# Optimization experiments

Hardware: AMD Instinct MI355X
Metric: run time of the kernel (lower is better)

Reference implementation:

```python
import jax, jax.numpy as jnp
import numpy as np

EMBED_DIM = 512
NUM_HEADS = 8
D_HEAD = EMBED_DIM // NUM_HEADS  # 64
BLOCK = 64
SEQ = 8192
BATCH = 2
N_GLOBAL = 2
N_WINDOW = 3
N_RANDOM = 3
NB = SEQ // BLOCK  # 128 blocks
M = N_GLOBAL + N_WINDOW + N_RANDOM  # gathered key blocks per query block


def setup_inputs() -> dict:
    key = jax.random.key(0)
    ks = jax.random.split(key, 12)
    s = 0.05  # ~xavier scale for [512,64]
    return {
        "query": jax.random.normal(ks[0], (SEQ, BATCH, EMBED_DIM), jnp.float32),
        "key_inp": jax.random.normal(ks[1], (SEQ, BATCH, EMBED_DIM), jnp.float32),
        "value": jax.random.normal(ks[2], (SEQ, BATCH, EMBED_DIM), jnp.float32),
        "q_w": jax.random.normal(ks[3], (NUM_HEADS, EMBED_DIM, D_HEAD), jnp.float32) * s,
        "k_w": jax.random.normal(ks[4], (NUM_HEADS, EMBED_DIM, D_HEAD), jnp.float32) * s,
        "v_w": jax.random.normal(ks[5], (NUM_HEADS, EMBED_DIM, D_HEAD), jnp.float32) * s,
        "q_b": jnp.zeros((NUM_HEADS, D_HEAD), jnp.float32),
        "k_b": jnp.zeros((NUM_HEADS, D_HEAD), jnp.float32),
        "v_b": jnp.zeros((NUM_HEADS, D_HEAD), jnp.float32),
        "out_w": jax.random.normal(ks[6], (EMBED_DIM, EMBED_DIM), jnp.float32) * 0.04,
        "out_b": jnp.zeros((EMBED_DIM,), jnp.float32),
        "rand_idx": jax.random.randint(ks[7], (NB, N_RANDOM), 0, NB, dtype=jnp.int32),
    }


def _gather_block_idx(rand_idx):
    # per query block: global blocks + sliding window (mod NB) + random blocks -> [NB, M]
    glob = jnp.broadcast_to(jnp.arange(N_GLOBAL, dtype=jnp.int32), (NB, N_GLOBAL))
    half = N_WINDOW // 2
    win = (jnp.arange(NB, dtype=jnp.int32)[:, None]
           + jnp.arange(N_WINDOW, dtype=jnp.int32)[None, :] - half) % NB
    return jnp.concatenate([glob, win, rand_idx], axis=1)


def _sparse_attn(Q, K, V, rand_idx):
    # Q,K,V: [B,H,S,dh] -> out [B,H,S,dh]
    B, H, S, dh = Q.shape
    Qb = Q.reshape(B, H, NB, BLOCK, dh)
    Kb = K.reshape(B, H, NB, BLOCK, dh)
    Vb = V.reshape(B, H, NB, BLOCK, dh)
    idx = _gather_block_idx(rand_idx)              # [NB, M]
    Kg = Kb[:, :, idx]                              # [B,H,NB,M,BLOCK,dh]
    Vg = Vb[:, :, idx].reshape(B, H, NB, M * BLOCK, dh)
    scores = jnp.einsum('bhnqd,bhnmkd->bhnqmk', Qb, Kg) / jnp.sqrt(jnp.float32(dh))
    scores = scores.reshape(B, H, NB, BLOCK, M * BLOCK)
    attn = jax.nn.softmax(scores, axis=-1)
    out = jnp.einsum('bhnqk,bhnkd->bhnqd', attn, Vg)
    return out.reshape(B, H, S, dh)


def reference(query, key_inp, value, q_w, k_w, v_w, q_b, k_b, v_b, out_w, out_b, rand_idx):
    # batch_first=False: [S,B,E] -> [B,S,E]
    q = jnp.transpose(query, (1, 0, 2))
    k = jnp.transpose(key_inp, (1, 0, 2))
    v = jnp.transpose(value, (1, 0, 2))
    # per-head projections: [B,S,E] x [H,E,dh] -> [B,H,S,dh]
    Q = jnp.einsum('bse,hed->bhsd', q, q_w) + q_b[None, :, None, :]
    K = jnp.einsum('bse,hed->bhsd', k, k_w) + k_b[None, :, None, :]
    V = jnp.einsum('bse,hed->bhsd', v, v_w) + v_b[None, :, None, :]
    ao = _sparse_attn(Q, K, V, rand_idx)            # [B,H,S,dh]
    flat = jnp.transpose(ao, (0, 2, 1, 3)).reshape(BATCH * SEQ, EMBED_DIM)
    out = flat @ out_w.T + out_b                    # nn.Linear
    out = out.reshape(BATCH, SEQ, EMBED_DIM)
    return jnp.transpose(out, (1, 0, 2))            # back to [S,B,E]
```

## Files before the change

kernel.cpp:

```cpp
#include <hip/hip_runtime.h>
#include <stdint.h>

#define NBLK 128
#define KDIM 512

typedef __attribute__((ext_vector_type(8))) short short8;
typedef __attribute__((ext_vector_type(4))) float f32x4;
typedef unsigned short u16;

__device__ __forceinline__ u16 f2bf(float f) {
  unsigned u = __float_as_uint(f);
  u = u + 0x7fffu + ((u >> 16) & 1u);
  return (u16)(u >> 16);
}

__device__ __forceinline__ short8 pack8(float4 a, float4 b) {
  short8 r;
  r[0] = (short)f2bf(a.x); r[1] = (short)f2bf(a.y);
  r[2] = (short)f2bf(a.z); r[3] = (short)f2bf(a.w);
  r[4] = (short)f2bf(b.x); r[5] = (short)f2bf(b.y);
  r[6] = (short)f2bf(b.z); r[7] = (short)f2bf(b.w);
  return r;
}

__device__ __forceinline__ void g2l16(const void* g, void* l) {
  __builtin_amdgcn_global_load_lds(
      (__attribute__((address_space(1))) void*)(g),
      (__attribute__((address_space(3))) void*)(l), 16, 0, 0);
}

__global__ void prep_weights(const float* __restrict__ qw, const float* __restrict__ kw,
                             const float* __restrict__ vw, const float* __restrict__ ow,
                             u16* __restrict__ wqt, u16* __restrict__ wkt,
                             u16* __restrict__ wvt, u16* __restrict__ owb) {
  int t = blockIdx.x * 256 + threadIdx.x;
  int y = blockIdx.y;
  if (y < 3) {
    const float* w = (y == 0) ? qw : (y == 1) ? kw : vw;
    u16* dstp = (y == 0) ? wqt : (y == 1) ? wkt : wvt;
    int c = t >> 7;
    int e4 = (t & 127) * 4;
    int h = c >> 6, d = c & 63;
    const float* base = w + h * (512 * 64) + d;
    ushort4 r;
    r.x = f2bf(base[(e4 + 0) * 64]);
    r.y = f2bf(base[(e4 + 1) * 64]);
    r.z = f2bf(base[(e4 + 2) * 64]);
    r.w = f2bf(base[(e4 + 3) * 64]);
    *(ushort4*)(dstp + c * 512 + e4) = r;
  } else {
    float4 val = *(const float4*)(ow + t * 4);
    ushort4 r;
    r.x = f2bf(val.x); r.y = f2bf(val.y); r.z = f2bf(val.z); r.w = f2bf(val.w);
    *(ushort4*)(owb + t * 4) = r;
  }
}

template <int MODE, bool AF32, bool BF32>
__device__ __forceinline__ void gemm_core(const void* __restrict__ Av, const void* __restrict__ Bv,
                                          const float* __restrict__ bias, void* __restrict__ dstv,
                                          int tileM, int tileN, u16* sh) {
  const int t = threadIdx.x;
  const int lane = t & 63, w = t >> 6;
  const int l15 = lane & 15, quad = lane >> 4;
  const int wm = w >> 1, wn = w & 1;
  u16* As = sh;
  u16* Bs = sh + 4096;

  f32x4 acc[4][4];
#pragma unroll
  for (int i = 0; i < 4; ++i)
#pragma unroll
    for (int j = 0; j < 4; ++j) acc[i][j] = (f32x4){0.f, 0.f, 0.f, 0.f};

  const int r = t >> 1, h = t & 1;
  const int swz = (r >> 1) & 3;

  const float* gA32 = nullptr; const u16* gA16 = nullptr;
  {
    const int grow = tileM + r;
    if (AF32) {
      const int b = grow >> 13, s = grow & 8191;
      gA32 = (const float*)Av + (size_t)(s * 2 + b) * 512 + h * 16;
    } else {
      gA16 = (const u16*)Av + (size_t)grow * 512 + h * 16;
    }
  }
  const float* gB32 = nullptr; const u16* gB16 = nullptr;
  {
    const int grow = tileN + r;
    if (BF32) {
      const int b = grow >> 13, s = grow & 8191;
      gB32 = (const float*)Bv + (size_t)(s * 2 + b) * 512 + h * 16;
    } else {
      gB16 = (const u16*)Bv + (size_t)grow * 512 + h * 16;
    }
  }

  u16* ldsA = As + r * 32;
  u16* ldsB = Bs + r * 32;
  const int p0 = ((2 * h) ^ swz) << 3;
  const int p1 = ((2 * h + 1) ^ swz) << 3;

  float4 fa[4], fb[4];
  short8 sa[2], sb[2];

#define LOAD_TILE(k0)                                             \
  do {                                                            \
    if (AF32) {                                                   \
      fa[0] = *(const float4*)(gA32 + (k0));                      \
      fa[1] = *(const float4*)(gA32 + (k0) + 4);                  \
      fa[2] = *(const float4*)(gA32 + (k0) + 8);                  \
      fa[3] = *(const float4*)(gA32 + (k0) + 12);                 \
    } else {                                                      \
      sa[0] = *(const short8*)(gA16 + (k0));                      \
      sa[1] = *(const short8*)(gA16 + (k0) + 8);                  \
    }                                                             \
    if (BF32) {                                                   \
      fb[0] = *(const float4*)(gB32 + (k0));                      \
      fb[1] = *(const float4*)(gB32 + (k0) + 4);                  \
      fb[2] = *(const float4*)(gB32 + (k0) + 8);                  \
      fb[3] = *(const float4*)(gB32 + (k0) + 12);                 \
    } else {                                                      \
      sb[0] = *(const short8*)(gB16 + (k0));                      \
      sb[1] = *(const short8*)(gB16 + (k0) + 8);                  \
    }                                                             \
  } while (0)

#define STORE_TILE()                                              \
  do {                                                            \
    if (AF32) {                                                   \
      *(short8*)(ldsA + p0) = pack8(fa[0], fa[1]);                \
      *(short8*)(ldsA + p1) = pack8(fa[2], fa[3]);                \
    } else {                                                      \
      *(short8*)(ldsA + p0) = sa[0];                              \
      *(short8*)(ldsA + p1) = sa[1];                              \
    }                                                             \
    if (BF32) {                                                   \
      *(short8*)(ldsB + p0) = pack8(fb[0], fb[1]);                \
      *(short8*)(ldsB + p1) = pack8(fb[2], fb[3]);                \
    } else {                                                      \
      *(short8*)(ldsB + p0) = sb[0];                              \
      *(short8*)(ldsB + p1) = sb[1];                              \
    }                                                             \
  } while (0)

  LOAD_TILE(0);
  STORE_TILE();
  __syncthreads();

  for (int k0 = 0; k0 < KDIM; k0 += 32) {
    const bool has_next = (k0 + 32 < KDIM);
    if (has_next) LOAD_TILE(k0 + 32);

    short8 af[4], bf[4];
#pragma unroll
    for (int mt = 0; mt < 4; ++mt) {
      const int ra = wm * 64 + mt * 16 + l15;
      af[mt] = *(const short8*)(As + ra * 32 + ((quad ^ ((ra >> 1) & 3)) << 3));
    }
#pragma unroll
    for (int nt = 0; nt < 4; ++nt) {
      const int rb = wn * 64 + nt * 16 + l15;
      bf[nt] = *(const short8*)(Bs + rb * 32 + ((quad ^ ((rb >> 1) & 3)) << 3));
    }
#pragma unroll
    for (int mt = 0; mt < 4; ++mt)
#pragma unroll
      for (int nt = 0; nt < 4; ++nt)
        acc[mt][nt] = __builtin_amdgcn_mfma_f32_16x16x32_bf16(af[mt], bf[nt], acc[mt][nt], 0, 0, 0);

    if (has_next) {
      __syncthreads();
      STORE_TILE();
      __syncthreads();
    }
  }
#undef LOAD_TILE
#undef STORE_TILE
  __syncthreads();

  if (MODE == 0 || MODE == 1) {
#pragma unroll
    for (int mt = 0; mt < 4; ++mt)
#pragma unroll
      for (int nt = 0; nt < 4; ++nt)
#pragma unroll
        for (int rr = 0; rr < 4; ++rr) {
          const int lrow = wm * 64 + mt * 16 + quad * 4 + rr;
          const int col = wn * 64 + nt * 16 + l15;
          float v = acc[mt][nt][rr] + (MODE == 0 ? bias[tileN + col] : bias[tileM + lrow]);
          const int ch = col >> 3;
          sh[lrow * 128 + ((ch ^ (lrow & 7)) << 3) + (col & 7)] = f2bf(v);
        }
    __syncthreads();
#pragma unroll
    for (int p = 0; p < 8; ++p) {
      const int idx = p * 256 + t;
      const int row = idx >> 4, c = idx & 15;
      short8 vch = *(const short8*)(sh + row * 128 + ((c ^ (row & 7)) << 3));
      if (MODE == 0) {
        const int m = tileM + row, b = m >> 13, s = m & 8191;
        const int n0 = tileN + c * 8, hh = n0 >> 6, d = n0 & 63;
        *(short8*)((u16*)dstv + (((b * 8 + hh) * 8192 + s) * 64 + d)) = vch;
      } else {
        const int hd = tileM + row;
        const int n0 = tileN + c * 8, b = n0 >> 13, s = n0 & 8191;
        *(short8*)((u16*)dstv + ((b * 512 + hd) * 8192 + s)) = vch;
      }
    }
  } else {
    float* Cf = (float*)sh;
#pragma unroll
    for (int half = 0; half < 2; ++half) {
      if (wm == half) {
#pragma unroll
        for (int mt = 0; mt < 4; ++mt)
#pragma unroll
          for (int nt = 0; nt < 4; ++nt)
#pragma unroll
            for (int rr = 0; rr < 4; ++rr) {
              const int lrow = mt * 16 + quad * 4 + rr;
              const int col = wn * 64 + nt * 16 + l15;
              float v = acc[mt][nt][rr] + bias[tileN + col];
              const int ch = col >> 2;
              Cf[lrow * 128 + ((ch ^ ((lrow & 7) << 2)) << 2) + (col & 3)] = v;
            }
      }
      __syncthreads();
#pragma unroll
      for (int p = 0; p < 8; ++p) {
        const int idx = p * 256 + t;
        const int row = idx >> 5, c = idx & 31;
        float4 v4 = *(const float4*)(Cf + row * 128 + ((c ^ ((row & 7) << 2)) << 2));
        const int m = tileM + half * 64 + row;
        const int s = m & 8191, b = m >> 13;
        *(float4*)((float*)dstv + ((s * 2 + b) * 512 + tileN + c * 4)) = v4;
      }
      __syncthreads();
    }
  }
}

__global__ __launch_bounds__(256, 4)
void gemm_qkv(const float* __restrict__ q, const float* __restrict__ k, const float* __restrict__ v,
              const u16* __restrict__ WqT, const u16* __restrict__ WkT, const u16* __restrict__ WvT,
              const float* __restrict__ qbi, const float* __restrict__ kbi, const float* __restrict__ vbi,
              u16* __restrict__ Qb, u16* __restrict__ Kb, u16* __restrict__ Vt) {
  __shared__ u16 sh[16384];
  const int id = blockIdx.x + blockIdx.y * 4;
  const int xs = (id >> 3) & 3;
  const int ys = (id & 7) * 16 + (id >> 5);
  const int z = blockIdx.z;
  if (z == 0)      gemm_core<0, true, false>(q, WqT, qbi, Qb, ys * 128, xs * 128, sh);
  else if (z == 1) gemm_core<0, true, false>(k, WkT, kbi, Kb, ys * 128, xs * 128, sh);
  else             gemm_core<1, false, true>(WvT, v, vbi, Vt, xs * 128, ys * 128, sh);
}

__global__ __launch_bounds__(256, 4)
void gemm_out_k(const u16* __restrict__ AO, const u16* __restrict__ OW,
                const float* __restrict__ ob, float* __restrict__ out) {
  __shared__ u16 sh[16384];
  const int id = blockIdx.x + blockIdx.y * 4;
  const int xs = (id >> 3) & 3;
  const int ys = (id & 7) * 16 + (id >> 5);
  gemm_core<2, false, false>(AO, OW, ob, out, ys * 128, xs * 128, sh);
}

__global__ __launch_bounds__(256, 5)
void attn(const u16* __restrict__ Qb, const u16* __restrict__ Kb,
          const u16* __restrict__ Vt, const int* __restrict__ ridx,
          u16* __restrict__ AO) {
  __shared__ u16 Ks[64 * 64];
  __shared__ u16 Vs[64 * 64];
  __shared__ u16 Ps[64 * 64];
  const int blk = blockIdx.x;
  const int bh = blk & 15, nb = blk >> 4;
  const int b = bh >> 3, h = bh & 7;
  const int t = threadIdx.x, lane = t & 63, w = t >> 6;
  const int l15 = lane & 15, quad = lane >> 4;

  int bidx[8];
  bidx[0] = 0; bidx[1] = 1;
  bidx[2] = (nb + NBLK - 1) & (NBLK - 1);
  bidx[3] = nb;
  bidx[4] = (nb + 1) & (NBLK - 1);
  bidx[5] = ridx[nb * 3 + 0];
  bidx[6] = ridx[nb * 3 + 1];
  bidx[7] = ridx[nb * 3 + 2];

  const u16* qrow = Qb + (bh * 8192 + nb * 64 + w * 16 + l15) * 64;
  short8 aq0 = *(const short8*)(qrow + quad * 8);
  short8 aq1 = *(const short8*)(qrow + 32 + quad * 8);

  const int s0 = t, s1 = t + 256;
  const int r0 = s0 >> 3, c0 = (s0 & 7) ^ (r0 & 7);
  const int r1 = s1 >> 3, c1 = (s1 & 7) ^ (r1 & 7);
  const u16* Kbase = Kb + bh * 8192 * 64;
  const u16* Vbase = Vt + (bh * 64) * 8192;

  f32x4 oacc[4];
#pragma unroll
  for (int i = 0; i < 4; ++i) oacc[i] = (f32x4){0.f, 0.f, 0.f, 0.f};
  float lsum[4] = {0.f, 0.f, 0.f, 0.f};

  for (int m = 0; m < 8; ++m) {
    const int kb0 = bidx[m] * 64;
    __syncthreads();
    g2l16(Kbase + (kb0 + r0) * 64 + c0 * 8, Ks + s0 * 8);
    g2l16(Kbase + (kb0 + r1) * 64 + c1 * 8, Ks + s1 * 8);
    g2l16(Vbase + r0 * 8192 + kb0 + c0 * 8, Vs + s0 * 8);
    g2l16(Vbase + r1 * 8192 + kb0 + c1 * 8, Vs + s1 * 8);
    __syncthreads();

    f32x4 s[4];
#pragma unroll
    for (int i = 0; i < 4; ++i) s[i] = (f32x4){0.f, 0.f, 0.f, 0.f};
#pragma unroll
    for (int nt = 0; nt < 4; ++nt) {
      const int key = nt * 16 + l15;
      const u16* kr = Ks + key * 64;
      short8 bk0 = *(const short8*)(kr + ((quad ^ (key & 7)) << 3));
      short8 bk1 = *(const short8*)(kr + (((4 + quad) ^ (key & 7)) << 3));
      s[nt] = __builtin_amdgcn_mfma_f32_16x16x32_bf16(aq0, bk0, s[nt], 0, 0, 0);
      s[nt] = __builtin_amdgcn_mfma_f32_16x16x32_bf16(aq1, bk1, s[nt], 0, 0, 0);
    }

#pragma unroll
    for (int nt = 0; nt < 4; ++nt) {
      const int key = nt * 16 + l15;
      const int cp = key >> 3;
#pragma unroll
      for (int rr = 0; rr < 4; ++rr) {
        float p = __expf(s[nt][rr] * 0.125f);
        lsum[rr] += p;
        const int q = w * 16 + quad * 4 + rr;
        Ps[q * 64 + (((cp ^ (q & 7)) << 3) | (key & 7))] = f2bf(p);
      }
    }

    const int q2 = w * 16 + l15;
    const u16* pr = Ps + q2 * 64;
    short8 ap0 = *(const short8*)(pr + ((quad ^ (q2 & 7)) << 3));
    short8 ap1 = *(const short8*)(pr + (((4 + quad) ^ (q2 & 7)) << 3));
#pragma unroll
    for (int nt = 0; nt < 4; ++nt) {
      const int d = nt * 16 + l15;
      const u16* vr = Vs + d * 64;
      short8 bv0 = *(const short8*)(vr + ((quad ^ (d & 7)) << 3));
      short8 bv1 = *(const short8*)(vr + (((4 + quad) ^ (d & 7)) << 3));
      oacc[nt] = __builtin_amdgcn_mfma_f32_16x16x32_bf16(ap0, bv0, oacc[nt], 0, 0, 0);
      oacc[nt] = __builtin_amdgcn_mfma_f32_16x16x32_bf16(ap1, bv1, oacc[nt], 0, 0, 0);
    }
  }

#pragma unroll
  for (int msk = 1; msk < 16; msk <<= 1)
#pragma unroll
    for (int rr = 0; rr < 4; ++rr) lsum[rr] += __shfl_xor(lsum[rr], msk, 64);
  float inv[4];
#pragma unroll
  for (int rr = 0; rr < 4; ++rr) inv[rr] = __builtin_amdgcn_rcpf(lsum[rr]);

#pragma unroll
  for (int nt = 0; nt < 4; ++nt) {
    const int cc = h * 64 + nt * 16 + l15;
#pragma unroll
    for (int rr = 0; rr < 4; ++rr) {
      const int s = nb * 64 + w * 16 + quad * 4 + rr;
      AO[(b * 8192 + s) * 512 + cc] = f2bf(oacc[nt][rr] * inv[rr]);
    }
  }
}

extern "C" void kernel_launch(void* const* d_in, const int* in_sizes, int n_in,
                              void* d_out, int out_size, void* d_ws, size_t ws_size,
                              hipStream_t stream) {
  const float* q   = (const float*)d_in[0];
  const float* k   = (const float*)d_in[1];
  const float* v   = (const float*)d_in[2];
  const float* qw  = (const float*)d_in[3];
  const float* kw  = (const float*)d_in[4];
  const float* vw  = (const float*)d_in[5];
  const float* qbi = (const float*)d_in[6];
  const float* kbi = (const float*)d_in[7];
  const float* vbi = (const float*)d_in[8];
  const float* ow  = (const float*)d_in[9];
  const float* ob  = (const float*)d_in[10];
  const int*   ri  = (const int*)d_in[11];

  char* ws = (char*)d_ws;
  const size_t MB1 = 1024 * 1024;
  u16* Qb   = (u16*)(ws + 0);
  u16* Kb   = (u16*)(ws + 16 * MB1);
  u16* Vt   = (u16*)(ws + 32 * MB1);
  u16* AO   = (u16*)(ws + 48 * MB1);
  u16* WqT  = (u16*)(ws + 64 * MB1);
  u16* WkT  = (u16*)(ws + 64 * MB1 + 512 * 1024);
  u16* WvT  = (u16*)(ws + 65 * MB1);
  u16* OW   = (u16*)(ws + 65 * MB1 + 512 * 1024);

  prep_weights<<<dim3(256, 4), 256, 0, stream>>>(qw, kw, vw, ow, WqT, WkT, WvT, OW);
  gemm_qkv<<<dim3(4, 128, 3), 256, 0, stream>>>(q, k, v, WqT, WkT, WvT,
                                                qbi, kbi, vbi, Qb, Kb, Vt);
  attn<<<2048, 256, 0, stream>>>(Qb, Kb, Vt, ri, AO);
  gemm_out_k<<<dim3(4, 128), 256, 0, stream>>>(AO, OW, ob, (float*)d_out);
}
```

Baseline: 254.3 us.

## Double-buffer LDS tiles in GEMM and attention kernels to overlap loads

The GEMM core now double-buffers its A/B tiles in LDS. It keeps two register sets so global loads run two k-steps ahead, and it drops to a single barrier per k-step. The attention kernel double-buffers its K/V blocks in LDS and prefetches the next gathered block while computing on the current one, again with one barrier per iteration. This aims to hide global-memory latency behind MFMA work, at the cost of more LDS and registers. Launch bounds are lowered by one wave group per kernel to make room, which may reduce occupancy.

Result: slower. 287.9 us (+13.2%).

```diff
diff --git a/kernel.cpp b/kernel.cpp
--- a/kernel.cpp
+++ b/kernel.cpp
@@ -64,8 +64,6 @@
   const int lane = t & 63, w = t >> 6;
   const int l15 = lane & 15, quad = lane >> 4;
   const int wm = w >> 1, wn = w & 1;
-  u16* As = sh;
-  u16* Bs = sh + 4096;
 
   f32x4 acc[4][4];
 #pragma unroll
@@ -97,72 +95,78 @@
     }
   }
 
-  u16* ldsA = As + r * 32;
-  u16* ldsB = Bs + r * 32;
+  u16* ldsA = sh + r * 32;
+  u16* ldsB = sh + 8192 + r * 32;
   const int p0 = ((2 * h) ^ swz) << 3;
   const int p1 = ((2 * h + 1) ^ swz) << 3;
 
-  float4 fa[4], fb[4];
-  short8 sa[2], sb[2];
-
-#define LOAD_TILE(k0)                                             \
+  float4 fa[2][4], fb[2][4];
+  short8 sa[2][2], sb[2][2];
+
+#define LOAD_TILE(k0, set)                                        \
   do {                                                            \
     if (AF32) {                                                   \
-      fa[0] = *(const float4*)(gA32 + (k0));                      \
-      fa[1] = *(const float4*)(gA32 + (k0) + 4);                  \
-      fa[2] = *(const float4*)(gA32 + (k0) + 8);                  \
-      fa[3] = *(const float4*)(gA32 + (k0) + 12);                 \
+      fa[set][0] = *(const float4*)(gA32 + (k0));                 \
+      fa[set][1] = *(const float4*)(gA32 + (k0) + 4);             \
+      fa[set][2] = *(const float4*)(gA32 + (k0) + 8);             \
+      fa[set][3] = *(const float4*)(gA32 + (k0) + 12);            \
     } else {                                                      \
-      sa[0] = *(const short8*)(gA16 + (k0));                      \
-      sa[1] = *(const short8*)(gA16 + (k0) + 8);                  \
+      sa[set][0] = *(const short8*)(gA16 + (k0));                 \
+      sa[set][1] = *(const short8*)(gA16 + (k0) + 8);             \
     }                                                             \
     if (BF32) {                                                   \
-      fb[0] = *(const float4*)(gB32 + (k0));                      \
-      fb[1] = *(const float4*)(gB32 + (k0) + 4);                  \
-      fb[2] = *(const float4*)(gB32 + (k0) + 8);                  \
-      fb[3] = *(const float4*)(gB32 + (k0) + 12);                 \
+      fb[set][0] = *(const float4*)(gB32 + (k0));                 \
+      fb[set][1] = *(const float4*)(gB32 + (k0) + 4);             \
+      fb[set][2] = *(const float4*)(gB32 + (k0) + 8);             \
+      fb[set][3] = *(const float4*)(gB32 + (k0) + 12);            \
     } else {                                                      \
-      sb[0] = *(const short8*)(gB16 + (k0));                      \
-      sb[1] = *(const short8*)(gB16 + (k0) + 8);                  \
+      sb[set][0] = *(const short8*)(gB16 + (k0));                 \
+      sb[set][1] = *(const short8*)(gB16 + (k0) + 8);             \
     }                                                             \
   } while (0)
 
-#define STORE_TILE()                                              \
+#define STORE_TILE(set, buf)                                      \
   do {                                                            \
+    u16* la = ldsA + (buf) * 4096;                                \
+    u16* lb = ldsB + (buf) * 4096;                                \
     if (AF32) {                                                   \
-      *(short8*)(ldsA + p0) = pack8(fa[0], fa[1]);                \
-      *(short8*)(ldsA + p1) = pack8(fa[2], fa[3]);                \
+      *(short8*)(la + p0) = pack8(fa[set][0], fa[set][1]);        \
+      *(short8*)(la + p1) = pack8(fa[set][2], fa[set][3]);        \
     } else {                                                      \
-      *(short8*)(ldsA + p0) = sa[0];                              \
-      *(short8*)(ldsA + p1) = sa[1];                              \
+      *(short8*)(la + p0) = sa[set][0];                           \
+      *(short8*)(la + p1) = sa[set][1];                           \
     }                                                             \
     if (BF32) {                                                   \
-      *(short8*)(ldsB + p0) = pack8(fb[0], fb[1]);                \
-      *(short8*)(ldsB + p1) = pack8(fb[2], fb[3]);                \
+      *(short8*)(lb + p0) = pack8(fb[set][0], fb[set][1]);        \
+      *(short8*)(lb + p1) = pack8(fb[set][2], fb[set][3]);        \
     } else {                                                      \
-      *(short8*)(ldsB + p0) = sb[0];                              \
-      *(short8*)(ldsB + p1) = sb[1];                              \
+      *(short8*)(lb + p0) = sb[set][0];                           \
+      *(short8*)(lb + p1) = sb[set][1];                           \
     }                                                             \
   } while (0)
 
-  LOAD_TILE(0);
-  STORE_TILE();
+  LOAD_TILE(0, 0);
+  STORE_TILE(0, 0);
+  LOAD_TILE(32, 1);
   __syncthreads();
 
-  for (int k0 = 0; k0 < KDIM; k0 += 32) {
-    const bool has_next = (k0 + 32 < KDIM);
-    if (has_next) LOAD_TILE(k0 + 32);
-
+#pragma unroll
+  for (int i = 0; i < 16; ++i) {
+    const int cur = i & 1;
+    if (i < 14) LOAD_TILE((i + 2) * 32, cur);
+
+    const u16* Ab = sh + cur * 4096;
+    const u16* Bb = sh + 8192 + cur * 4096;
     short8 af[4], bf[4];
 #pragma unroll
     for (int mt = 0; mt < 4; ++mt) {
       const int ra = wm * 64 + mt * 16 + l15;
-      af[mt] = *(const short8*)(As + ra * 32 + ((quad ^ ((ra >> 1) & 3)) << 3));
+      af[mt] = *(const short8*)(Ab + ra * 32 + ((quad ^ ((ra >> 1) & 3)) << 3));
     }
 #pragma unroll
     for (int nt = 0; nt < 4; ++nt) {
       const int rb = wn * 64 + nt * 16 + l15;
-      bf[nt] = *(const short8*)(Bs + rb * 32 + ((quad ^ ((rb >> 1) & 3)) << 3));
+      bf[nt] = *(const short8*)(Bb + rb * 32 + ((quad ^ ((rb >> 1) & 3)) << 3));
     }
 #pragma unroll
     for (int mt = 0; mt < 4; ++mt)
@@ -170,15 +174,11 @@
       for (int nt = 0; nt < 4; ++nt)
         acc[mt][nt] = __builtin_amdgcn_mfma_f32_16x16x32_bf16(af[mt], bf[nt], acc[mt][nt], 0, 0, 0);
 
-    if (has_next) {
-      __syncthreads();
-      STORE_TILE();
-      __syncthreads();
-    }
+    if (i < 15) STORE_TILE((i + 1) & 1, (i + 1) & 1);
+    __syncthreads();
   }
 #undef LOAD_TILE
 #undef STORE_TILE
-  __syncthreads();
 
   if (MODE == 0 || MODE == 1) {
 #pragma unroll
@@ -242,7 +242,7 @@
   }
 }
 
-__global__ __launch_bounds__(256, 4)
+__global__ __launch_bounds__(256, 3)
 void gemm_qkv(const float* __restrict__ q, const float* __restrict__ k, const float* __restrict__ v,
               const u16* __restrict__ WqT, const u16* __restrict__ WkT, const u16* __restrict__ WvT,
               const float* __restrict__ qbi, const float* __restrict__ kbi, const float* __restrict__ vbi,
@@ -257,7 +257,7 @@
   else             gemm_core<1, false, true>(WvT, v, vbi, Vt, xs * 128, ys * 128, sh);
 }
 
-__global__ __launch_bounds__(256, 4)
+__global__ __launch_bounds__(256, 3)
 void gemm_out_k(const u16* __restrict__ AO, const u16* __restrict__ OW,
                 const float* __restrict__ ob, float* __restrict__ out) {
   __shared__ u16 sh[16384];
@@ -267,12 +267,12 @@
   gemm_core<2, false, false>(AO, OW, ob, out, ys * 128, xs * 128, sh);
 }
 
-__global__ __launch_bounds__(256, 5)
+__global__ __launch_bounds__(256, 4)
 void attn(const u16* __restrict__ Qb, const u16* __restrict__ Kb,
           const u16* __restrict__ Vt, const int* __restrict__ ridx,
           u16* __restrict__ AO) {
-  __shared__ u16 Ks[64 * 64];
-  __shared__ u16 Vs[64 * 64];
+  __shared__ u16 Ks[2][64 * 64];
+  __shared__ u16 Vs[2][64 * 64];
   __shared__ u16 Ps[64 * 64];
   const int blk = blockIdx.x;
   const int bh = blk & 15, nb = blk >> 4;
@@ -299,19 +299,27 @@
   const u16* Kbase = Kb + bh * 8192 * 64;
   const u16* Vbase = Vt + (bh * 64) * 8192;
 
+#define STAGE_KV(m, buf)                                               \
+  do {                                                                 \
+    const int kb0 = bidx[m] * 64;                                      \
+    g2l16(Kbase + (kb0 + r0) * 64 + c0 * 8, Ks[buf] + s0 * 8);         \
+    g2l16(Kbase + (kb0 + r1) * 64 + c1 * 8, Ks[buf] + s1 * 8);         \
+    g2l16(Vbase + r0 * 8192 + kb0 + c0 * 8, Vs[buf] + s0 * 8);         \
+    g2l16(Vbase + r1 * 8192 + kb0 + c1 * 8, Vs[buf] + s1 * 8);         \
+  } while (0)
+
   f32x4 oacc[4];
 #pragma unroll
   for (int i = 0; i < 4; ++i) oacc[i] = (f32x4){0.f, 0.f, 0.f, 0.f};
   float lsum[4] = {0.f, 0.f, 0.f, 0.f};
 
+  STAGE_KV(0, 0);
+  __syncthreads();
+
+#pragma unroll
   for (int m = 0; m < 8; ++m) {
-    const int kb0 = bidx[m] * 64;
-    __syncthreads();
-    g2l16(Kbase + (kb0 + r0) * 64 + c0 * 8, Ks + s0 * 8);
-    g2l16(Kbase + (kb0 + r1) * 64 + c1 * 8, Ks + s1 * 8);
-    g2l16(Vbase + r0 * 8192 + kb0 + c0 * 8, Vs + s0 * 8);
-    g2l16(Vbase + r1 * 8192 + kb0 + c1 * 8, Vs + s1 * 8);
-    __syncthreads();
+    const int cur = m & 1;
+    if (m < 7) STAGE_KV(m + 1, cur ^ 1);
 
     f32x4 s[4];
 #pragma unroll
@@ -319,7 +327,7 @@
 #pragma unroll
     for (int nt = 0; nt < 4; ++nt) {
       const int key = nt * 16 + l15;
-      const u16* kr = Ks + key * 64;
+      const u16* kr = Ks[cur] + key * 64;
       short8 bk0 = *(const short8*)(kr + ((quad ^ (key & 7)) << 3));
       short8 bk1 = *(const short8*)(kr + (((4 + quad) ^ (key & 7)) << 3));
       s[nt] = __builtin_amdgcn_mfma_f32_16x16x32_bf16(aq0, bk0, s[nt], 0, 0, 0);
@@ -346,13 +354,15 @@
 #pragma unroll
     for (int nt = 0; nt < 4; ++nt) {
       const int d = nt * 16 + l15;
-      const u16* vr = Vs + d * 64;
+      const u16* vr = Vs[cur] + d * 64;
       short8 bv0 = *(const short8*)(vr + ((quad ^ (d & 7)) << 3));
       short8 bv1 = *(const short8*)(vr + (((4 + quad) ^ (d & 7)) << 3));
       oacc[nt] = __builtin_amdgcn_mfma_f32_16x16x32_bf16(ap0, bv0, oacc[nt], 0, 0, 0);
       oacc[nt] = __builtin_amdgcn_mfma_f32_16x16x32_bf16(ap1, bv1, oacc[nt], 0, 0, 0);
     }
-  }
+    __syncthreads();
+  }
+#undef STAGE_KV
 
 #pragma unroll
   for (int msk = 1; msk < 16; msk <<= 1)
```

## Load GEMM tiles directly into LDS via global_load_lds, convert fp32 at fragment read

Applied to the files above, without the earlier changes.

Replaces the register-staged global loads and LDS stores with asynchronous global_load_lds transfers, keeping fp32 activations in LDS (with an XOR swizzle) and converting them to bf16 only when forming MFMA fragments. The simpler bf16-to-bf16 rounding replaces round-to-nearest-even with a round-half-up add. This removes the register software-pipelining (prefetch of the next tile), so loads are no longer overlapped with compute and each k-step now waits on two barriers around the transfer. It also doubles LDS traffic for fp32 operands and repeats the conversion per wave.

Measured after the change: 250.3 us. No clear change (-1.6%).

```diff
diff --git a/kernel.cpp b/kernel.cpp
--- a/kernel.cpp
+++ b/kernel.cpp
@@ -14,12 +14,12 @@
   return (u16)(u >> 16);
 }
 
-__device__ __forceinline__ short8 pack8(float4 a, float4 b) {
+__device__ __forceinline__ short8 pack_ru(f32x4 a, f32x4 b) {
   short8 r;
-  r[0] = (short)f2bf(a.x); r[1] = (short)f2bf(a.y);
-  r[2] = (short)f2bf(a.z); r[3] = (short)f2bf(a.w);
-  r[4] = (short)f2bf(b.x); r[5] = (short)f2bf(b.y);
-  r[6] = (short)f2bf(b.z); r[7] = (short)f2bf(b.w);
+#pragma unroll
+  for (int i = 0; i < 4; ++i) r[i] = (short)((__float_as_uint(a[i]) + 0x8000u) >> 16);
+#pragma unroll
+  for (int i = 0; i < 4; ++i) r[4 + i] = (short)((__float_as_uint(b[i]) + 0x8000u) >> 16);
   return r;
 }
 
@@ -64,8 +64,7 @@
   const int lane = t & 63, w = t >> 6;
   const int l15 = lane & 15, quad = lane >> 4;
   const int wm = w >> 1, wn = w & 1;
-  u16* As = sh;
-  u16* Bs = sh + 4096;
+  const int BOFF = AF32 ? 8192 : 4096;
 
   f32x4 acc[4][4];
 #pragma unroll
@@ -73,111 +72,92 @@
 #pragma unroll
     for (int j = 0; j < 4; ++j) acc[i][j] = (f32x4){0.f, 0.f, 0.f, 0.f};
 
-  const int r = t >> 1, h = t & 1;
-  const int swz = (r >> 1) & 3;
-
-  const float* gA32 = nullptr; const u16* gA16 = nullptr;
-  {
-    const int grow = tileM + r;
+  const float* aSrcF[4]; const u16* aSrcH[2];
+  if (AF32) {
+#pragma unroll
+    for (int i = 0; i < 4; ++i) {
+      const int s = t + i * 256;
+      const int r = s >> 3, g = (s & 7) ^ (r & 7);
+      const int grow = tileM + r;
+      const int bb = grow >> 13, ss = grow & 8191;
+      aSrcF[i] = (const float*)Av + (size_t)(ss * 2 + bb) * 512 + g * 4;
+    }
+  } else {
+#pragma unroll
+    for (int i = 0; i < 2; ++i) {
+      const int s = t + i * 256;
+      const int r = s >> 2, g = (s & 3) ^ ((r >> 1) & 3);
+      aSrcH[i] = (const u16*)Av + (size_t)(tileM + r) * 512 + g * 8;
+    }
+  }
+  const float* bSrcF[4]; const u16* bSrcH[2];
+  if (BF32) {
+#pragma unroll
+    for (int i = 0; i < 4; ++i) {
+      const int s = t + i * 256;
+      const int r = s >> 3, g = (s & 7) ^ (r & 7);
+      const int grow = tileN + r;
+      const int bb = grow >> 13, ss = grow & 8191;
+      bSrcF[i] = (const float*)Bv + (size_t)(ss * 2 + bb) * 512 + g * 4;
+    }
+  } else {
+#pragma unroll
+    for (int i = 0; i < 2; ++i) {
+      const int s = t + i * 256;
+      const int r = s >> 2, g = (s & 3) ^ ((r >> 1) & 3);
+      bSrcH[i] = (const u16*)Bv + (size_t)(tileN + r) * 512 + g * 8;
+    }
+  }
+
+  for (int k0 = 0; k0 < KDIM; k0 += 32) {
+    __syncthreads();
     if (AF32) {
-      const int b = grow >> 13, s = grow & 8191;
-      gA32 = (const float*)Av + (size_t)(s * 2 + b) * 512 + h * 16;
+#pragma unroll
+      for (int i = 0; i < 4; ++i) g2l16(aSrcF[i] + k0, sh + (t + i * 256) * 8);
     } else {
-      gA16 = (const u16*)Av + (size_t)grow * 512 + h * 16;
-    }
-  }
-  const float* gB32 = nullptr; const u16* gB16 = nullptr;
-  {
-    const int grow = tileN + r;
+#pragma unroll
+      for (int i = 0; i < 2; ++i) g2l16(aSrcH[i] + k0, sh + (t + i * 256) * 8);
+    }
     if (BF32) {
-      const int b = grow >> 13, s = grow & 8191;
-      gB32 = (const float*)Bv + (size_t)(s * 2 + b) * 512 + h * 16;
+#pragma unroll
+      for (int i = 0; i < 4; ++i) g2l16(bSrcF[i] + k0, sh + BOFF + (t + i * 256) * 8);
     } else {
-      gB16 = (const u16*)Bv + (size_t)grow * 512 + h * 16;
-    }
-  }
-
-  u16* ldsA = As + r * 32;
-  u16* ldsB = Bs + r * 32;
-  const int p0 = ((2 * h) ^ swz) << 3;
-  const int p1 = ((2 * h + 1) ^ swz) << 3;
-
-  float4 fa[4], fb[4];
-  short8 sa[2], sb[2];
-
-#define LOAD_TILE(k0)                                             \
-  do {                                                            \
-    if (AF32) {                                                   \
-      fa[0] = *(const float4*)(gA32 + (k0));                      \
-      fa[1] = *(const float4*)(gA32 + (k0) + 4);                  \
-      fa[2] = *(const float4*)(gA32 + (k0) + 8);                  \
-      fa[3] = *(const float4*)(gA32 + (k0) + 12);                 \
-    } else {                                                      \
-      sa[0] = *(const short8*)(gA16 + (k0));                      \
-      sa[1] = *(const short8*)(gA16 + (k0) + 8);                  \
-    }                                                             \
-    if (BF32) {                                                   \
-      fb[0] = *(const float4*)(gB32 + (k0));                      \
-      fb[1] = *(const float4*)(gB32 + (k0) + 4);                  \
-      fb[2] = *(const float4*)(gB32 + (k0) + 8);                  \
-      fb[3] = *(const float4*)(gB32 + (k0) + 12);                 \
-    } else {                                                      \
-      sb[0] = *(const short8*)(gB16 + (k0));                      \
-      sb[1] = *(const short8*)(gB16 + (k0) + 8);                  \
-    }                                                             \
-  } while (0)
-
-#define STORE_TILE()                                              \
-  do {                                                            \
-    if (AF32) {                                                   \
-      *(short8*)(ldsA + p0) = pack8(fa[0], fa[1]);                \
-      *(short8*)(ldsA + p1) = pack8(fa[2], fa[3]);                \
-    } else {                                                      \
-      *(short8*)(ldsA + p0) = sa[0];                              \
-      *(short8*)(ldsA + p1) = sa[1];                              \
-    }                                                             \
-    if (BF32) {                                                   \
-      *(short8*)(ldsB + p0) = pack8(fb[0], fb[1]);                \
-      *(short8*)(ldsB + p1) = pack8(fb[2], fb[3]);                \
-    } else {                                                      \
-      *(short8*)(ldsB + p0) = sb[0];                              \
-      *(short8*)(ldsB + p1) = sb[1];                              \
-    }                                                             \
-  } while (0)
-
-  LOAD_TILE(0);
-  STORE_TILE();
-  __syncthreads();
-
-  for (int k0 = 0; k0 < KDIM; k0 += 32) {
-    const bool has_next = (k0 + 32 < KDIM);
-    if (has_next) LOAD_TILE(k0 + 32);
+#pragma unroll
+      for (int i = 0; i < 2; ++i) g2l16(bSrcH[i] + k0, sh + BOFF + (t + i * 256) * 8);
+    }
+    __syncthreads();
 
     short8 af[4], bf[4];
 #pragma unroll
     for (int mt = 0; mt < 4; ++mt) {
       const int ra = wm * 64 + mt * 16 + l15;
-      af[mt] = *(const short8*)(As + ra * 32 + ((quad ^ ((ra >> 1) & 3)) << 3));
+      if (AF32) {
+        const float* Af = (const float*)sh;
+        f32x4 f0 = *(const f32x4*)(Af + ra * 32 + (((2 * quad) ^ (ra & 7)) << 2));
+        f32x4 f1 = *(const f32x4*)(Af + ra * 32 + (((2 * quad + 1) ^ (ra & 7)) << 2));
+        af[mt] = pack_ru(f0, f1);
+      } else {
+        af[mt] = *(const short8*)(sh + ra * 32 + ((quad ^ ((ra >> 1) & 3)) << 3));
+      }
     }
 #pragma unroll
     for (int nt = 0; nt < 4; ++nt) {
       const int rb = wn * 64 + nt * 16 + l15;
-      bf[nt] = *(const short8*)(Bs + rb * 32 + ((quad ^ ((rb >> 1) & 3)) << 3));
+      if (BF32) {
+        const float* Bf = (const float*)(sh + BOFF);
+        f32x4 f0 = *(const f32x4*)(Bf + rb * 32 + (((2 * quad) ^ (rb & 7)) << 2));
+        f32x4 f1 = *(const f32x4*)(Bf + rb * 32 + (((2 * quad + 1) ^ (rb & 7)) << 2));
+        bf[nt] = pack_ru(f0, f1);
+      } else {
+        bf[nt] = *(const short8*)(sh + BOFF + rb * 32 + ((quad ^ ((rb >> 1) & 3)) << 3));
+      }
     }
 #pragma unroll
     for (int mt = 0; mt < 4; ++mt)
 #pragma unroll
       for (int nt = 0; nt < 4; ++nt)
         acc[mt][nt] = __builtin_amdgcn_mfma_f32_16x16x32_bf16(af[mt], bf[nt], acc[mt][nt], 0, 0, 0);
-
-    if (has_next) {
-      __syncthreads();
-      STORE_TILE();
-      __syncthreads();
-    }
-  }
-#undef LOAD_TILE
-#undef STORE_TILE
+  }
   __syncthreads();
 
   if (MODE == 0 || MODE == 1) {
@@ -247,7 +227,7 @@
               const u16* __restrict__ WqT, const u16* __restrict__ WkT, const u16* __restrict__ WvT,
               const float* __restrict__ qbi, const float* __restrict__ kbi, const float* __restrict__ vbi,
               u16* __restrict__ Qb, u16* __restrict__ Kb, u16* __restrict__ Vt) {
-  __shared__ u16 sh[16384];
+  __shared__ __align__(16) u16 sh[16384];
   const int id = blockIdx.x + blockIdx.y * 4;
   const int xs = (id >> 3) & 3;
   const int ys = (id & 7) * 16 + (id >> 5);
@@ -260,7 +240,7 @@
 __global__ __launch_bounds__(256, 4)
 void gemm_out_k(const u16* __restrict__ AO, const u16* __restrict__ OW,
                 const float* __restrict__ ob, float* __restrict__ out) {
-  __shared__ u16 sh[16384];
+  __shared__ __align__(16) u16 sh[16384];
   const int id = blockIdx.x + blockIdx.y * 4;
   const int xs = (id >> 3) & 3;
   const int ys = (id & 7) * 16 + (id >> 5);
```
